# Optimization experiments

Measured on AMD Instinct MI355X. Metric: run time of the kernel, lower is better.

The kernel has to match this reference:

```python
import jax, jax.numpy as jnp
import numpy as np
import math

B, T, D = 2, 2048, 2048
H = 16
HD = D // H
FF = D * 2


def rmsnorm(x, w):
    eps = jnp.finfo(x.dtype).eps  # torch RMSNorm default eps=None -> finfo eps
    ms = jnp.mean(jnp.square(x), axis=-1, keepdims=True)
    return x * jax.lax.rsqrt(ms + eps) * w


def setup_inputs() -> dict:
    key = jax.random.key(0)
    ks = jax.random.split(key, 8)
    s = 0.02
    return {
        "x": jax.random.normal(ks[0], (B, T, D), jnp.float32),
        "scale_gamma": jax.random.uniform(ks[1], (D,), jnp.float32, 0.5, 1.5),
        "scale_beta": jax.random.normal(ks[2], (D,), jnp.float32) * 0.1,
        "qkv_w": jax.random.normal(ks[3], (3 * D, D), jnp.float32) * s,
        "o_w": jax.random.normal(ks[4], (D, D), jnp.float32) * s,
        "gate_w": jax.random.normal(ks[5], (FF, D), jnp.float32) * s,
        "up_w": jax.random.normal(ks[6], (FF, D), jnp.float32) * s,
        "down_w": jax.random.normal(ks[7], (D, FF), jnp.float32) * s,
        "norm1_w": jnp.ones((D,), jnp.float32),
        "norm2_w": jnp.ones((D,), jnp.float32),
    }


def reference(x, scale_gamma, scale_beta, qkv_w, o_w, gate_w, up_w, down_w, norm1_w, norm2_w):
    # --- attention sub-block ---
    h = rmsnorm(x, norm1_w) * scale_gamma + scale_beta
    qkv = (h @ qkv_w.T).reshape(B, T, 3, H, HD)
    q, k, v = [jnp.transpose(qkv[:, :, i], (0, 2, 1, 3)) for i in range(3)]  # (B,H,T,HD)
    scores = jnp.einsum("bhqd,bhkd->bhqk", q, k) / math.sqrt(HD)
    causal = jnp.tril(jnp.ones((T, T), bool))
    scores = jnp.where(causal, scores, -jnp.inf)
    attn = jax.nn.softmax(scores, axis=-1)
    out = jnp.einsum("bhqk,bhkd->bhqd", attn, v)
    out = jnp.transpose(out, (0, 2, 1, 3)).reshape(B, T, D)
    x = x + out @ o_w.T
    # --- SwiGLU FFN sub-block ---
    h = rmsnorm(x, norm2_w) * scale_gamma + scale_beta
    ff = jax.nn.silu(h @ gate_w.T) * (h @ up_w.T)
    return x + ff @ down_w.T
```

## Files before the change

kernel.cpp:

```cpp
#include <hip/hip_runtime.h>
#include <cstdint>

#define D_MODEL 2048
#define T_SEQ   2048
#define BATCH   2
#define NHEAD   16
#define HDIM    128
#define FFDIM   4096
#define NTOK    4096

using bf16_t = __bf16;
typedef __attribute__((ext_vector_type(8))) __bf16 bf16x8;
typedef __attribute__((ext_vector_type(4))) __bf16 bf16x4;
typedef __attribute__((ext_vector_type(4))) float  f32x4;

typedef __attribute__((address_space(1))) void as1_void;
typedef __attribute__((address_space(3))) void as3_void;

__device__ __forceinline__ void async_copy16(const void* g, void* lds) {
  __builtin_amdgcn_global_load_lds((as1_void*)(uintptr_t)g,
                                   (as3_void*)(uint32_t)(uintptr_t)lds,
                                   16, 0, 0);
}

__device__ __forceinline__ void barrier_raw() {
  asm volatile("s_barrier" ::: "memory");
}

__device__ __forceinline__ size_t packidx(int n, int kc, int nkt) {
  int kt = kc >> 2, kg = kc & 3;
  return (((size_t)(n >> 7) * nkt + kt) << 9) + (kg << 7) + (n & 127);
}

#define NQ 1572864
#define NO 524288
#define NG 1048576
#define NU 1048576
#define ND 1048576
#define TOTC (NQ + NO + NG + NU + ND)
__global__ __launch_bounds__(256) void f2b_all_kernel(
    const float* __restrict__ s0, const float* __restrict__ s1,
    const float* __restrict__ s2, const float* __restrict__ s3,
    const float* __restrict__ s4,
    bf16_t* __restrict__ d0, bf16_t* __restrict__ d1,
    bf16_t* __restrict__ dgu, bf16_t* __restrict__ d4) {
  int c = blockIdx.x * 256 + threadIdx.x;
  const int stride = gridDim.x * 256;
  for (; c < TOTC; c += stride) {
    const float* src; bf16_t* dst; size_t didx; int sf4;
    if (c < NQ) {
      int n = c >> 8, kc = c & 255;
      src = s0; sf4 = n * 512 + kc * 2;
      dst = d0; didx = packidx(n, kc, 64);
    } else if (c < NQ + NO) {
      int lc = c - NQ, n = lc >> 8, kc = lc & 255;
      src = s1; sf4 = n * 512 + kc * 2;
      dst = d1; didx = packidx(n, kc, 64);
    } else if (c < NQ + NO + NG) {
      int lc = c - NQ - NO, g = lc >> 8, kc = lc & 255;
      int n2 = ((g >> 4) << 5) + (g & 15);
      src = s2; sf4 = g * 512 + kc * 2;
      dst = dgu; didx = packidx(n2, kc, 64);
    } else if (c < NQ + NO + NG + NU) {
      int lc = c - NQ - NO - NG, u = lc >> 8, kc = lc & 255;
      int n2 = ((u >> 4) << 5) + 16 + (u & 15);
      src = s3; sf4 = u * 512 + kc * 2;
      dst = dgu; didx = packidx(n2, kc, 64);
    } else {
      int lc = c - NQ - NO - NG - NU, n = lc >> 9, kc = lc & 511;
      src = s4; sf4 = n * 1024 + kc * 2;
      dst = d4; didx = packidx(n, kc, 128);
    }
    float4 v0 = ((const float4*)src)[sf4];
    float4 v1 = ((const float4*)src)[sf4 + 1];
    bf16x8 r;
    r[0] = (bf16_t)v0.x; r[1] = (bf16_t)v0.y; r[2] = (bf16_t)v0.z; r[3] = (bf16_t)v0.w;
    r[4] = (bf16_t)v1.x; r[5] = (bf16_t)v1.y; r[6] = (bf16_t)v1.z; r[7] = (bf16_t)v1.w;
    *(bf16x8*)(dst + didx * 8) = r;
  }
}

__global__ __launch_bounds__(256) void rmsnorm_kernel(const float* __restrict__ x,
                                                      const float* __restrict__ nw,
                                                      const float* __restrict__ gamma,
                                                      const float* __restrict__ beta,
                                                      bf16_t* __restrict__ out) {
  const int row = blockIdx.x;
  const int t = threadIdx.x;
  const float* xr = x + (size_t)row * D_MODEL;
  float4 va = ((const float4*)xr)[2 * t];
  float4 vb = ((const float4*)xr)[2 * t + 1];
  float ss = va.x*va.x + va.y*va.y + va.z*va.z + va.w*va.w
           + vb.x*vb.x + vb.y*vb.y + vb.z*vb.z + vb.w*vb.w;
#pragma unroll
  for (int off = 1; off < 64; off <<= 1) ss += __shfl_xor(ss, off, 64);
  __shared__ float sred[4];
  if ((t & 63) == 0) sred[t >> 6] = ss;
  __syncthreads();
  float tot = sred[0] + sred[1] + sred[2] + sred[3];
  float inv = rsqrtf(tot * (1.0f / D_MODEL) + 1.1920929e-07f);
  const int c0 = t * 8;
  float a8[8] = {va.x, va.y, va.z, va.w, vb.x, vb.y, vb.z, vb.w};
  bf16x8 r;
#pragma unroll
  for (int j = 0; j < 8; ++j)
    r[j] = (bf16_t)(a8[j] * inv * nw[c0 + j] * gamma[c0 + j] + beta[c0 + j]);
  *(bf16x8*)(out + packidx(row, t, 64) * 8) = r;
}

template <int EPI>
__global__ __launch_bounds__(512, 2) void gemm256_kernel(
    const bf16_t* __restrict__ A, const bf16_t* __restrict__ Bw,
    int M, int N, int K, void* out) {
  __shared__ alignas(16) char ldsbuf[131072];
  const int tid = threadIdx.x;
  const int wave = tid >> 6, lane = tid & 63;
  const int quad = lane >> 4, l16 = lane & 15;
  const int wm = wave >> 2, wn = wave & 3;

  const int bx = blockIdx.x, by = blockIdx.y;

  const int nk = K >> 5;
  const char* pA0 = (const char*)A  + (((size_t)(2 * by)     * nk) << 13) + tid * 16;
  const char* pA1 = (const char*)A  + (((size_t)(2 * by + 1) * nk) << 13) + tid * 16;
  const char* pB0 = (const char*)Bw + (((size_t)(2 * bx)     * nk) << 13) + tid * 16;
  const char* pB1 = (const char*)Bw + (((size_t)(2 * bx + 1) * nk) << 13) + tid * 16;

  auto stageA = [&](int b) {
    async_copy16(pA0, ldsbuf + (b << 15) + wave * 1024);
    async_copy16(pA1, ldsbuf + (b << 15) + 8192 + wave * 1024);
    pA0 += 8192; pA1 += 8192;
  };
  auto stageB = [&](int b) {
    async_copy16(pB0, ldsbuf + (b << 15) + 16384 + wave * 1024);
    async_copy16(pB1, ldsbuf + (b << 15) + 24576 + wave * 1024);
    pB0 += 8192; pB1 += 8192;
  };

  const f32x4 fzero = {0.f, 0.f, 0.f, 0.f};
  f32x4 acc[8][4];
#pragma unroll
  for (int i = 0; i < 8; ++i)
#pragma unroll
    for (int j = 0; j < 4; ++j) acc[i][j] = fzero;

  stageA(0); stageB(0); stageA(1); stageB(1); stageA(2); stageB(2);
  asm volatile("s_waitcnt vmcnt(8)" ::: "memory");
  barrier_raw();

  for (int j = 0; j < nk; ++j) {
    const int b = j & 3;
    const int bs = (b + 3) & 3;
    const bool more = (j + 3 < nk);
    const char* Ab = ldsbuf + (b << 15) + (wm << 13) + (quad << 11);
    const char* Bb = ldsbuf + (b << 15) + 16384 + ((wn >> 1) << 13) + (quad << 11) +
                     ((wn & 1) << 10);
    bf16x8 af[4], bfr[4];
#pragma unroll
    for (int mi = 0; mi < 4; ++mi)
      af[mi] = *(const bf16x8*)(Ab + (mi * 16 + l16) * 16);
#pragma unroll
    for (int ni = 0; ni < 4; ++ni)
      bfr[ni] = *(const bf16x8*)(Bb + (ni * 16 + l16) * 16);
    if (more) stageA(bs);
    barrier_raw();
    __builtin_amdgcn_s_setprio(1);
#pragma unroll
    for (int mi = 0; mi < 4; ++mi)
#pragma unroll
      for (int ni = 0; ni < 4; ++ni)
        acc[mi][ni] = __builtin_amdgcn_mfma_f32_16x16x32_bf16(af[mi], bfr[ni],
                                                              acc[mi][ni], 0, 0, 0);
    __builtin_amdgcn_s_setprio(0);
    barrier_raw();
#pragma unroll
    for (int mi = 0; mi < 4; ++mi)
      af[mi] = *(const bf16x8*)(Ab + ((mi + 4) * 16 + l16) * 16);
    if (more) stageB(bs);
    barrier_raw();
    __builtin_amdgcn_s_setprio(1);
#pragma unroll
    for (int mi = 0; mi < 4; ++mi)
#pragma unroll
      for (int ni = 0; ni < 4; ++ni)
        acc[mi + 4][ni] = __builtin_amdgcn_mfma_f32_16x16x32_bf16(af[mi], bfr[ni],
                                                                  acc[mi + 4][ni], 0, 0, 0);
    __builtin_amdgcn_s_setprio(0);
    if (j + 3 < nk)      asm volatile("s_waitcnt vmcnt(8)" ::: "memory");
    else if (j + 2 < nk) asm volatile("s_waitcnt vmcnt(4)" ::: "memory");
    else if (j + 1 < nk) asm volatile("s_waitcnt vmcnt(0)" ::: "memory");
    barrier_raw();
  }

  const int rowbase = by * 256 + wm * 128;
  const int colbase = bx * 256 + wn * 64;
  if (EPI == 4) {
#pragma unroll
    for (int mi = 0; mi < 8; ++mi) {
#pragma unroll
      for (int r = 0; r < 4; ++r) {
        const int row = rowbase + mi * 16 + quad * 4 + r;
        const int rt = row >> 7, m = row & 127;
#pragma unroll
        for (int p = 0; p < 2; ++p) {
          float g = acc[mi][2 * p][r];
          float u = acc[mi][2 * p + 1][r];
          float sv = g / (1.0f + __expf(-g));
          const int ffcol = (bx * 8 + wn * 2 + p) * 16 + l16;
          const int kt2 = ffcol >> 5, kg2 = (ffcol >> 3) & 3, e = ffcol & 7;
          const size_t idx =
              (((((size_t)rt * 128 + kt2) << 9) + (kg2 << 7) + m) << 3) + e;
          ((bf16_t*)out)[idx] = (bf16_t)(sv * u);
        }
      }
    }
  } else {
#pragma unroll
    for (int mi = 0; mi < 8; ++mi) {
#pragma unroll
      for (int r = 0; r < 4; ++r) {
        const int row = rowbase + mi * 16 + quad * 4 + r;
        const size_t base = (size_t)row * N;
#pragma unroll
        for (int ni = 0; ni < 4; ++ni) {
          const int col = colbase + ni * 16 + l16;
          ((bf16_t*)out)[base + col] = (bf16_t)acc[mi][ni][r];
        }
      }
    }
  }
}

template <int EPI>
__global__ __launch_bounds__(256) void gemm_kernel(const bf16_t* __restrict__ A,
                                                   const bf16_t* __restrict__ Bw,
                                                   int M, int N, int K,
                                                   void* out, const void* aux) {
  __shared__ alignas(16) bf16_t As[2][4][128][8];
  __shared__ alignas(16) bf16_t Bs[2][4][128][8];
  const int tid = threadIdx.x;
  const int wave = tid >> 6, lane = tid & 63;
  const int quad = lane >> 4, l16 = lane & 15;
  const int bx = blockIdx.x, by = blockIdx.y;
  const int wr = (wave >> 1) * 64, wc = (wave & 1) * 64;
  const int rowA0 = by * 128, colB0 = bx * 128;

  const f32x4 fzero = {0.f, 0.f, 0.f, 0.f};
  f32x4 acc[4][4];
#pragma unroll
  for (int i = 0; i < 4; ++i)
#pragma unroll
    for (int j = 0; j < 4; ++j) acc[i][j] = fzero;

  const int nk = K >> 5;
  const bf16_t* a0 = A + ((size_t)by * nk << 12) + tid * 8;
  const bf16_t* a1 = a0 + 2048;
  const bf16_t* b0 = Bw + ((size_t)bx * nk << 12) + tid * 8;
  const bf16_t* b1 = b0 + 2048;
  char* ldsA0 = (char*)As + (wave * 64) * 16;
  char* ldsA1 = (char*)As + (256 + wave * 64) * 16;
  char* ldsB0 = (char*)Bs + (wave * 64) * 16;
  char* ldsB1 = (char*)Bs + (256 + wave * 64) * 16;

  async_copy16(a0, ldsA0);
  async_copy16(a1, ldsA1);
  async_copy16(b0, ldsB0);
  async_copy16(b1, ldsB1);
  a0 += 4096; a1 += 4096; b0 += 4096; b1 += 4096;

  for (int kt = 0; kt < nk; ++kt) {
    __syncthreads();
    const int cur = kt & 1;
    if (kt + 1 < nk) {
      const int nxt = 8192 * (1 - cur);
      async_copy16(a0, ldsA0 + nxt);
      async_copy16(a1, ldsA1 + nxt);
      async_copy16(b0, ldsB0 + nxt);
      async_copy16(b1, ldsB1 + nxt);
      a0 += 4096; a1 += 4096; b0 += 4096; b1 += 4096;
    }
    bf16x8 af[4], bfr[4];
#pragma unroll
    for (int mi = 0; mi < 4; ++mi)
      af[mi] = *(const bf16x8*)&As[cur][quad][wr + mi * 16 + l16][0];
#pragma unroll
    for (int ni = 0; ni < 4; ++ni)
      bfr[ni] = *(const bf16x8*)&Bs[cur][quad][wc + ni * 16 + l16][0];
#pragma unroll
    for (int mi = 0; mi < 4; ++mi)
#pragma unroll
      for (int ni = 0; ni < 4; ++ni)
        acc[mi][ni] = __builtin_amdgcn_mfma_f32_16x16x32_bf16(af[mi], bfr[ni],
                                                              acc[mi][ni], 0, 0, 0);
  }

#pragma unroll
  for (int mi = 0; mi < 4; ++mi) {
#pragma unroll
    for (int r = 0; r < 4; ++r) {
      const int row = rowA0 + wr + mi * 16 + quad * 4 + r;
      const size_t base = (size_t)row * N;
#pragma unroll
      for (int ni = 0; ni < 4; ++ni) {
        const int col = colB0 + wc + ni * 16 + l16;
        const size_t idx = base + col;
        float v = acc[mi][ni][r];
        if (EPI == 0) {
          ((bf16_t*)out)[idx] = (bf16_t)v;
        } else {
          ((float*)out)[idx] = v + ((const float*)aux)[idx];
        }
      }
    }
  }
}

__global__ __launch_bounds__(256) void vtrans_kernel(const bf16_t* __restrict__ qkv,
                                                     bf16_t* __restrict__ vt) {
  const int bh = blockIdx.y;
  const int b = bh >> 4, h = bh & 15;
  const int t0 = blockIdx.x << 6;
  const int tid = threadIdx.x;
  __shared__ bf16_t tile[64][136];
#pragma unroll
  for (int r = 0; r < 4; ++r) {
    int ci = r * 256 + tid;
    int t = ci >> 4, dc = ci & 15;
    bf16x8 v = *(const bf16x8*)(qkv + (size_t)(b * T_SEQ + t0 + t) * 6144 + 4096 +
                                h * HDIM + dc * 8);
    *(bf16x8*)&tile[t][dc * 8] = v;
  }
  __syncthreads();
#pragma unroll
  for (int r = 0; r < 4; ++r) {
    int ci = r * 256 + tid;
    int d = ci >> 3, ts = ci & 7;
    bf16x8 o;
#pragma unroll
    for (int j = 0; j < 8; ++j) o[j] = tile[ts * 8 + j][d];
    *(bf16x8*)(vt + ((size_t)bh * HDIM + d) * T_SEQ + t0 + ts * 8) = o;
  }
}

__global__ __launch_bounds__(256) void attn_kernel(const bf16_t* __restrict__ qkv,
                                                   const bf16_t* __restrict__ vt,
                                                   bf16_t* __restrict__ out) {
  const int bh = blockIdx.y;
  const int b = bh >> 4, h = bh & 15;
  const int qt = gridDim.x - 1 - blockIdx.x;
  const int q0 = qt << 6;
  const int tid = threadIdx.x;
  const int wave = tid >> 6, lane = tid & 63;
  const int quad = lane >> 4, l16 = lane & 15;

  __shared__ alignas(16) bf16_t Ks[2][64 * 128];
  __shared__ alignas(16) bf16_t VTs[2][128 * 64];
  __shared__ bf16_t Ps[4][16][68];

  const size_t qbase = (size_t)(b * T_SEQ + q0 + wave * 16 + l16) * 6144 + h * HDIM;
  bf16x8 qf[4];
#pragma unroll
  for (int kk = 0; kk < 4; ++kk)
    qf[kk] = *(const bf16x8*)(qkv + qbase + kk * 32 + quad * 8);

  const bf16_t* gK[4];
  const bf16_t* gV[4];
#pragma unroll
  for (int c = 0; c < 4; ++c) {
    int ci = c * 256 + tid;
    int t = ci >> 4, dcs = ci & 15;
    int dc = dcs ^ (t & 15);
    gK[c] = qkv + (size_t)(b * T_SEQ + t) * 6144 + 2048 + h * HDIM + dc * 8;
    int d = ci >> 3, tcs = ci & 7;
    int tc = tcs ^ (d & 7);
    gV[c] = vt + ((size_t)bh * HDIM + d) * T_SEQ + tc * 8;
  }
  char* ldsK = (char*)Ks + wave * 1024;
  char* ldsV = (char*)VTs + wave * 1024;

  auto stage = [&](int buf) {
#pragma unroll
    for (int c = 0; c < 4; ++c) {
      async_copy16(gK[c], ldsK + buf * 16384 + c * 4096);
      gK[c] += 64 * 6144;
    }
#pragma unroll
    for (int c = 0; c < 4; ++c) {
      async_copy16(gV[c], ldsV + buf * 16384 + c * 4096);
      gV[c] += 64;
    }
  };

  const f32x4 fzero = {0.f, 0.f, 0.f, 0.f};
  f32x4 o[8];
#pragma unroll
  for (int i = 0; i < 8; ++i) o[i] = fzero;
  float mrow[4]  = {-3.0e38f, -3.0e38f, -3.0e38f, -3.0e38f};
  float lpart[4] = {0.f, 0.f, 0.f, 0.f};

  const float sc = 0.08838834764831845f;
  const float THR = 8.0f;
  const int ktmax = qt;

  stage(0);

  for (int kt = 0; kt <= ktmax; ++kt) {
    const int cur = kt & 1;
    __syncthreads();
    if (kt < ktmax) stage(1 - cur);

    const bf16_t* Kc = &Ks[cur][0];
    const bf16_t* Vc = &VTs[cur][0];

    f32x4 s[4];
#pragma unroll
    for (int nt = 0; nt < 4; ++nt) {
      s[nt] = fzero;
#pragma unroll
      for (int kk = 0; kk < 4; ++kk) {
        int tK = nt * 16 + l16;
        int cK = kk * 4 + quad;
        bf16x8 kf = *(const bf16x8*)(Kc + (tK * 16 + (cK ^ l16)) * 8);
        s[nt] = __builtin_amdgcn_mfma_f32_16x16x32_bf16(qf[kk], kf, s[nt], 0, 0, 0);
      }
    }

    const int qr0 = q0 + wave * 16 + quad * 4;
    const bool diag = (kt == ktmax);
    float pmax[4];
#pragma unroll
    for (int r = 0; r < 4; ++r) {
      const int qr = qr0 + r;
      float mx = -3.0e38f;
#pragma unroll
      for (int nt = 0; nt < 4; ++nt) {
        float v = s[nt][r] * sc;
        if (diag) {
          int kc = kt * 64 + nt * 16 + l16;
          v = (kc <= qr) ? v : -3.0e38f;
        }
        s[nt][r] = v;
        mx = fmaxf(mx, v);
      }
      pmax[r] = mx;
    }
    bool ok = (pmax[0] <= mrow[0] + THR) & (pmax[1] <= mrow[1] + THR) &
              (pmax[2] <= mrow[2] + THR) & (pmax[3] <= mrow[3] + THR);
    if (!__all(ok)) {
      float alpha[4];
#pragma unroll
      for (int r = 0; r < 4; ++r) {
        float mx = pmax[r];
#pragma unroll
        for (int off = 1; off < 16; off <<= 1) mx = fmaxf(mx, __shfl_xor(mx, off, 16));
        float mnew = fmaxf(mrow[r], mx);
        alpha[r] = __expf(mrow[r] - mnew);
        mrow[r] = mnew;
        lpart[r] *= alpha[r];
      }
#pragma unroll
      for (int i = 0; i < 8; ++i)
#pragma unroll
        for (int r = 0; r < 4; ++r) o[i][r] *= alpha[r];
    }
#pragma unroll
    for (int r = 0; r < 4; ++r) {
#pragma unroll
      for (int nt = 0; nt < 4; ++nt) {
        float pv = __expf(s[nt][r] - mrow[r]);
        s[nt][r] = pv;
        lpart[r] += pv;
      }
    }
#pragma unroll
    for (int nt = 0; nt < 4; ++nt)
#pragma unroll
      for (int r = 0; r < 4; ++r)
        Ps[wave][quad * 4 + r][nt * 16 + l16] = (bf16_t)s[nt][r];

#pragma unroll
    for (int kk2 = 0; kk2 < 2; ++kk2) {
      const bf16_t* prow = &Ps[wave][l16][kk2 * 32 + quad * 8];
      bf16x4 p0 = *(const bf16x4*)prow;
      bf16x4 p1 = *(const bf16x4*)(prow + 4);
      bf16x8 pf;
#pragma unroll
      for (int j = 0; j < 4; ++j) { pf[j] = p0[j]; pf[4 + j] = p1[j]; }
#pragma unroll
      for (int nt2 = 0; nt2 < 8; ++nt2) {
        int dV = nt2 * 16 + l16;
        int tcV = kk2 * 4 + quad;
        bf16x8 vf = *(const bf16x8*)(Vc + (dV * 8 + (tcV ^ (dV & 7))) * 8);
        o[nt2] = __builtin_amdgcn_mfma_f32_16x16x32_bf16(pf, vf, o[nt2], 0, 0, 0);
      }
    }
  }

  float rl[4];
#pragma unroll
  for (int r = 0; r < 4; ++r) {
    float l = lpart[r];
#pragma unroll
    for (int off = 1; off < 16; off <<= 1) l += __shfl_xor(l, off, 16);
    rl[r] = 1.0f / l;
  }
#pragma unroll
  for (int nt2 = 0; nt2 < 8; ++nt2) {
#pragma unroll
    for (int r = 0; r < 4; ++r) {
      const int gt = b * T_SEQ + q0 + wave * 16 + quad * 4 + r;
      const int mt = gt >> 7, m = gt & 127;
      const int col = h * HDIM + nt2 * 16 + l16;
      const int kt2 = col >> 5, kg2 = (col >> 3) & 3, e = col & 7;
      const size_t idx = (((((size_t)mt * 64 + kt2) << 9) + (kg2 << 7) + m) << 3) + e;
      out[idx] = (bf16_t)(o[nt2][r] * rl[r]);
    }
  }
}

extern "C" void kernel_launch(void* const* d_in, const int* in_sizes, int n_in,
                              void* d_out, int out_size, void* d_ws, size_t ws_size,
                              hipStream_t stream) {
  const float* x      = (const float*)d_in[0];
  const float* gamma  = (const float*)d_in[1];
  const float* beta   = (const float*)d_in[2];
  const float* qkv_w  = (const float*)d_in[3];
  const float* o_w    = (const float*)d_in[4];
  const float* gate_w = (const float*)d_in[5];
  const float* up_w   = (const float*)d_in[6];
  const float* down_w = (const float*)d_in[7];
  const float* n1w    = (const float*)d_in[8];
  const float* n2w    = (const float*)d_in[9];
  float* out = (float*)d_out;

  char* p = (char*)d_ws;
  bf16_t* qkv_wb  = (bf16_t*)p; p += (size_t)3 * D_MODEL * D_MODEL * 2;
  bf16_t* o_wb    = (bf16_t*)p; p += (size_t)D_MODEL * D_MODEL * 2;
  bf16_t* gu_wb   = (bf16_t*)p; p += (size_t)2 * FFDIM * D_MODEL * 2;
  bf16_t* down_wb = (bf16_t*)p; p += (size_t)D_MODEL * FFDIM * 2;
  bf16_t* h_b     = (bf16_t*)p; p += (size_t)NTOK * D_MODEL * 2;
  bf16_t* qkv_b   = (bf16_t*)p; p += (size_t)NTOK * 3 * D_MODEL * 2;
  bf16_t* attn_b  = (bf16_t*)p; p += (size_t)NTOK * D_MODEL * 2;
  float*  x1      = (float*)p;  p += (size_t)NTOK * D_MODEL * 4;
  bf16_t* g_b     = (bf16_t*)p; p += (size_t)NTOK * FFDIM * 2;
  bf16_t* vt_b    = g_b;

  dim3 blk(256);
  dim3 blk512(512);
  f2b_all_kernel<<<dim3(2048), blk, 0, stream>>>(
      qkv_w, o_w, gate_w, up_w, down_w,
      qkv_wb, o_wb, gu_wb, down_wb);

  rmsnorm_kernel<<<dim3(NTOK), blk, 0, stream>>>(x, n1w, gamma, beta, h_b);
  gemm256_kernel<0><<<dim3(3 * D_MODEL / 256, NTOK / 256), blk512, 0, stream>>>(
      h_b, qkv_wb, NTOK, 3 * D_MODEL, D_MODEL, qkv_b);
  vtrans_kernel<<<dim3(T_SEQ / 64, BATCH * NHEAD), blk, 0, stream>>>(qkv_b, vt_b);
  attn_kernel<<<dim3(T_SEQ / 64, BATCH * NHEAD), blk, 0, stream>>>(qkv_b, vt_b, attn_b);
  gemm_kernel<1><<<dim3(D_MODEL / 128, NTOK / 128), blk, 0, stream>>>(
      attn_b, o_wb, NTOK, D_MODEL, D_MODEL, x1, x);

  rmsnorm_kernel<<<dim3(NTOK), blk, 0, stream>>>(x1, n2w, gamma, beta, h_b);
  gemm256_kernel<4><<<dim3(2 * FFDIM / 256, NTOK / 256), blk512, 0, stream>>>(
      h_b, gu_wb, NTOK, 2 * FFDIM, D_MODEL, g_b);
  gemm_kernel<1><<<dim3(D_MODEL / 128, NTOK / 128), blk, 0, stream>>>(
      g_b, down_wb, NTOK, D_MODEL, FFDIM, out, x1);
}
```

Baseline: 825.5 us.

## Software-pipeline LDS fragment loads in GEMM main loop and halve barriers

Restructures the bf16 MFMA GEMM main loop. The next tile's A-low and B fragments are prefetched from LDS into double-buffered registers, so the reads overlap the second MFMA half of the current tile. The per-iteration barriers drop from four to two, and the vmcnt wait moves to before the prefetch. The loop is unrolled by two to alternate the register buffers. This assumes an even number of K tiles and raises register pressure.

```diff
diff --git a/kernel.cpp b/kernel.cpp
--- a/kernel.cpp
+++ b/kernel.cpp
@@ -137,59 +137,77 @@
     pB0 += 8192; pB1 += 8192;
   };
 
+  const int aoff = (wm << 13) + (quad << 11);
+  const int boff = 16384 + ((wn >> 1) << 13) + (quad << 11) + ((wn & 1) << 10);
+
   const f32x4 fzero = {0.f, 0.f, 0.f, 0.f};
   f32x4 acc[8][4];
 #pragma unroll
   for (int i = 0; i < 8; ++i)
 #pragma unroll
     for (int j = 0; j < 4; ++j) acc[i][j] = fzero;
+
+  bf16x8 afLo[4], afHi[4], bfr0[4], bfr1[4];
 
   stageA(0); stageB(0); stageA(1); stageB(1); stageA(2); stageB(2);
   asm volatile("s_waitcnt vmcnt(8)" ::: "memory");
   barrier_raw();
-
-  for (int j = 0; j < nk; ++j) {
-    const int b = j & 3;
-    const int bs = (b + 3) & 3;
-    const bool more = (j + 3 < nk);
-    const char* Ab = ldsbuf + (b << 15) + (wm << 13) + (quad << 11);
-    const char* Bb = ldsbuf + (b << 15) + 16384 + ((wn >> 1) << 13) + (quad << 11) +
-                     ((wn & 1) << 10);
-    bf16x8 af[4], bfr[4];
+  {
+    const char* Ab = ldsbuf + aoff;
+    const char* Bb = ldsbuf + boff;
 #pragma unroll
     for (int mi = 0; mi < 4; ++mi)
-      af[mi] = *(const bf16x8*)(Ab + (mi * 16 + l16) * 16);
+      afLo[mi] = *(const bf16x8*)(Ab + (mi * 16 + l16) * 16);
 #pragma unroll
     for (int ni = 0; ni < 4; ++ni)
-      bfr[ni] = *(const bf16x8*)(Bb + (ni * 16 + l16) * 16);
-    if (more) stageA(bs);
-    barrier_raw();
+      bfr0[ni] = *(const bf16x8*)(Bb + (ni * 16 + l16) * 16);
+  }
+
+  auto tile_step = [&](int j, bf16x8 (&bCur)[4], bf16x8 (&bNxt)[4]) {
+    const int b = j & 3, bs = (j + 3) & 3, bn = (j + 1) & 3;
+    const bool more3 = (j + 3 < nk);
+    const char* Ab = ldsbuf + (b << 15) + aoff;
+    if (more3) stageA(bs);
+#pragma unroll
+    for (int mi = 0; mi < 4; ++mi)
+      afHi[mi] = *(const bf16x8*)(Ab + ((mi + 4) * 16 + l16) * 16);
     __builtin_amdgcn_s_setprio(1);
 #pragma unroll
     for (int mi = 0; mi < 4; ++mi)
 #pragma unroll
       for (int ni = 0; ni < 4; ++ni)
-        acc[mi][ni] = __builtin_amdgcn_mfma_f32_16x16x32_bf16(af[mi], bfr[ni],
+        acc[mi][ni] = __builtin_amdgcn_mfma_f32_16x16x32_bf16(afLo[mi], bCur[ni],
                                                               acc[mi][ni], 0, 0, 0);
     __builtin_amdgcn_s_setprio(0);
-    barrier_raw();
-#pragma unroll
-    for (int mi = 0; mi < 4; ++mi)
-      af[mi] = *(const bf16x8*)(Ab + ((mi + 4) * 16 + l16) * 16);
-    if (more) stageB(bs);
-    barrier_raw();
-    __builtin_amdgcn_s_setprio(1);
-#pragma unroll
-    for (int mi = 0; mi < 4; ++mi)
-#pragma unroll
-      for (int ni = 0; ni < 4; ++ni)
-        acc[mi + 4][ni] = __builtin_amdgcn_mfma_f32_16x16x32_bf16(af[mi], bfr[ni],
-                                                                  acc[mi + 4][ni], 0, 0, 0);
-    __builtin_amdgcn_s_setprio(0);
-    if (j + 3 < nk)      asm volatile("s_waitcnt vmcnt(8)" ::: "memory");
+    if (more3)           asm volatile("s_waitcnt vmcnt(6)" ::: "memory");
     else if (j + 2 < nk) asm volatile("s_waitcnt vmcnt(4)" ::: "memory");
     else if (j + 1 < nk) asm volatile("s_waitcnt vmcnt(0)" ::: "memory");
     barrier_raw();
+    if (more3) stageB(bs);
+    if (j + 1 < nk) {
+      const char* An = ldsbuf + (bn << 15) + aoff;
+      const char* Bn = ldsbuf + (bn << 15) + boff;
+#pragma unroll
+      for (int mi = 0; mi < 4; ++mi)
+        afLo[mi] = *(const bf16x8*)(An + (mi * 16 + l16) * 16);
+#pragma unroll
+      for (int ni = 0; ni < 4; ++ni)
+        bNxt[ni] = *(const bf16x8*)(Bn + (ni * 16 + l16) * 16);
+    }
+    __builtin_amdgcn_s_setprio(1);
+#pragma unroll
+    for (int mi = 0; mi < 4; ++mi)
+#pragma unroll
+      for (int ni = 0; ni < 4; ++ni)
+        acc[mi + 4][ni] = __builtin_amdgcn_mfma_f32_16x16x32_bf16(afHi[mi], bCur[ni],
+                                                                  acc[mi + 4][ni], 0, 0, 0);
+    __builtin_amdgcn_s_setprio(0);
+    barrier_raw();
+  };
+
+  for (int j = 0; j < nk; j += 2) {
+    tile_step(j,     bfr0, bfr1);
+    tile_step(j + 1, bfr1, bfr0);
   }
 
   const int rowbase = by * 256 + wm * 128;
```

Measured after the change: 824.6 us. No clear change (-0.1%).

## Drop intra-iteration barriers and interleave async copies with MFMA chunks in GEMM

Applied to the files above, without the earlier changes.

Restructures the 256x256 GEMM main loop so each K-step issues its four async global-to-LDS copies spread across four MFMA chunks. It drops two of the three workgroup barriers per iteration and relies on the 4-deep buffer ring with prefetch distance 3 for safety. sched_barrier calls pin the instruction interleaving. The aim is to cut barrier stalls and overlap memory issue with matrix math. The cost is B-fragment loads split into halves, plus tighter dependence on the compiler honouring the schedule.

```diff
diff --git a/kernel.cpp b/kernel.cpp
--- a/kernel.cpp
+++ b/kernel.cpp
@@ -126,16 +126,8 @@
   const char* pB0 = (const char*)Bw + (((size_t)(2 * bx)     * nk) << 13) + tid * 16;
   const char* pB1 = (const char*)Bw + (((size_t)(2 * bx + 1) * nk) << 13) + tid * 16;
 
-  auto stageA = [&](int b) {
-    async_copy16(pA0, ldsbuf + (b << 15) + wave * 1024);
-    async_copy16(pA1, ldsbuf + (b << 15) + 8192 + wave * 1024);
-    pA0 += 8192; pA1 += 8192;
-  };
-  auto stageB = [&](int b) {
-    async_copy16(pB0, ldsbuf + (b << 15) + 16384 + wave * 1024);
-    async_copy16(pB1, ldsbuf + (b << 15) + 24576 + wave * 1024);
-    pB0 += 8192; pB1 += 8192;
-  };
+  const int aoff = (wm << 13) + (quad << 11);
+  const int boff = 16384 + ((wn >> 1) << 13) + (quad << 11) + ((wn & 1) << 10);
 
   const f32x4 fzero = {0.f, 0.f, 0.f, 0.f};
   f32x4 acc[8][4];
@@ -144,51 +136,78 @@
 #pragma unroll
     for (int j = 0; j < 4; ++j) acc[i][j] = fzero;
 
-  stageA(0); stageB(0); stageA(1); stageB(1); stageA(2); stageB(2);
+#pragma unroll
+  for (int t0 = 0; t0 < 3; ++t0) {
+    char* d = ldsbuf + (t0 << 15) + wave * 1024;
+    async_copy16(pA0, d);          pA0 += 8192;
+    async_copy16(pA1, d + 8192);   pA1 += 8192;
+    async_copy16(pB0, d + 16384);  pB0 += 8192;
+    async_copy16(pB1, d + 24576);  pB1 += 8192;
+  }
   asm volatile("s_waitcnt vmcnt(8)" ::: "memory");
   barrier_raw();
 
-  for (int j = 0; j < nk; ++j) {
-    const int b = j & 3;
-    const int bs = (b + 3) & 3;
-    const bool more = (j + 3 < nk);
-    const char* Ab = ldsbuf + (b << 15) + (wm << 13) + (quad << 11);
-    const char* Bb = ldsbuf + (b << 15) + 16384 + ((wn >> 1) << 13) + (quad << 11) +
-                     ((wn & 1) << 10);
-    bf16x8 af[4], bfr[4];
+  for (int t = 0; t < nk; ++t) {
+    const int b = t & 3, bs = (t + 3) & 3;
+    const bool more = (t + 3 < nk);
+    const char* Ab = ldsbuf + (b << 15) + aoff;
+    const char* Bb = ldsbuf + (b << 15) + boff;
+    char* dst = ldsbuf + (bs << 15) + wave * 1024;
+    bf16x8 af[4], bf[4];
+    if (more) { async_copy16(pA0, dst); pA0 += 8192; }
 #pragma unroll
     for (int mi = 0; mi < 4; ++mi)
       af[mi] = *(const bf16x8*)(Ab + (mi * 16 + l16) * 16);
 #pragma unroll
-    for (int ni = 0; ni < 4; ++ni)
-      bfr[ni] = *(const bf16x8*)(Bb + (ni * 16 + l16) * 16);
-    if (more) stageA(bs);
-    barrier_raw();
+    for (int ni = 0; ni < 2; ++ni)
+      bf[ni] = *(const bf16x8*)(Bb + (ni * 16 + l16) * 16);
     __builtin_amdgcn_s_setprio(1);
 #pragma unroll
     for (int mi = 0; mi < 4; ++mi)
 #pragma unroll
-      for (int ni = 0; ni < 4; ++ni)
-        acc[mi][ni] = __builtin_amdgcn_mfma_f32_16x16x32_bf16(af[mi], bfr[ni],
+      for (int ni = 0; ni < 2; ++ni)
+        acc[mi][ni] = __builtin_amdgcn_mfma_f32_16x16x32_bf16(af[mi], bf[ni],
                                                               acc[mi][ni], 0, 0, 0);
     __builtin_amdgcn_s_setprio(0);
-    barrier_raw();
+    __builtin_amdgcn_sched_barrier(0);
+    if (more) { async_copy16(pA1, dst + 8192); pA1 += 8192; }
+#pragma unroll
+    for (int ni = 2; ni < 4; ++ni)
+      bf[ni] = *(const bf16x8*)(Bb + (ni * 16 + l16) * 16);
+    __builtin_amdgcn_s_setprio(1);
+#pragma unroll
+    for (int mi = 0; mi < 4; ++mi)
+#pragma unroll
+      for (int ni = 2; ni < 4; ++ni)
+        acc[mi][ni] = __builtin_amdgcn_mfma_f32_16x16x32_bf16(af[mi], bf[ni],
+                                                              acc[mi][ni], 0, 0, 0);
+    __builtin_amdgcn_s_setprio(0);
+    __builtin_amdgcn_sched_barrier(0);
+    if (more) { async_copy16(pB0, dst + 16384); pB0 += 8192; }
 #pragma unroll
     for (int mi = 0; mi < 4; ++mi)
       af[mi] = *(const bf16x8*)(Ab + ((mi + 4) * 16 + l16) * 16);
-    if (more) stageB(bs);
-    barrier_raw();
     __builtin_amdgcn_s_setprio(1);
 #pragma unroll
     for (int mi = 0; mi < 4; ++mi)
 #pragma unroll
-      for (int ni = 0; ni < 4; ++ni)
-        acc[mi + 4][ni] = __builtin_amdgcn_mfma_f32_16x16x32_bf16(af[mi], bfr[ni],
+      for (int ni = 0; ni < 2; ++ni)
+        acc[mi + 4][ni] = __builtin_amdgcn_mfma_f32_16x16x32_bf16(af[mi], bf[ni],
                                                                   acc[mi + 4][ni], 0, 0, 0);
     __builtin_amdgcn_s_setprio(0);
-    if (j + 3 < nk)      asm volatile("s_waitcnt vmcnt(8)" ::: "memory");
-    else if (j + 2 < nk) asm volatile("s_waitcnt vmcnt(4)" ::: "memory");
-    else if (j + 1 < nk) asm volatile("s_waitcnt vmcnt(0)" ::: "memory");
+    __builtin_amdgcn_sched_barrier(0);
+    if (more) { async_copy16(pB1, dst + 24576); pB1 += 8192; }
+    __builtin_amdgcn_s_setprio(1);
+#pragma unroll
+    for (int mi = 0; mi < 4; ++mi)
+#pragma unroll
+      for (int ni = 2; ni < 4; ++ni)
+        acc[mi + 4][ni] = __builtin_amdgcn_mfma_f32_16x16x32_bf16(af[mi], bf[ni],
+                                                                  acc[mi + 4][ni], 0, 0, 0);
+    __builtin_amdgcn_s_setprio(0);
+    if (more)            asm volatile("s_waitcnt vmcnt(8)" ::: "memory");
+    else if (t + 2 < nk) asm volatile("s_waitcnt vmcnt(4)" ::: "memory");
+    else if (t + 1 < nk) asm volatile("s_waitcnt vmcnt(0)" ::: "memory");
     barrier_raw();
   }
 
```

Result: no change. 819.7 us (-0.7%).
